# Performance work log

Measured on AMD Instinct MI355X. Metric: run time of the kernel, lower is better.

The kernel has to match this reference:

```python
import jax, jax.numpy as jnp
import numpy as np


def phi(x):
    # ELU + 1 feature map (Katharopoulos et al. 2020)
    return jax.nn.elu(x) + 1.0


def setup_inputs() -> dict:
    key = jax.random.key(0)
    k1, k2, k3 = jax.random.split(key, 3)
    B, T, D = 2, 2048, 512
    x = jax.random.normal(k1, (B, T, D), dtype=jnp.float32)
    # torch nn.Linear stores weight as (out_features, in_features)
    w_qkv = jax.random.normal(k2, (3 * D, D), dtype=jnp.float32) * 0.02
    w_out = jax.random.normal(k3, (D, D), dtype=jnp.float32) * 0.02
    return {"x": x, "w_qkv": w_qkv, "w_out": w_out, "n_heads": 16}


def reference(x, w_qkv, w_out, n_heads):
    B, T, D = x.shape
    H = n_heads
    Dh = D // H
    qkv = x @ w_qkv.T                                   # (B,T,3D)
    qkv = qkv.reshape(B, T, 3, H, Dh).transpose(2, 0, 3, 1, 4)  # (3,B,H,T,Dh)
    q, k, v = phi(qkv[0]), phi(qkv[1]), qkv[2]
    # kv outer product: (B,H,T,Dh_k,Dh_v), causal cumsum over time
    kv = k[..., :, None] * v[..., None, :]
    kv_cumsum = jnp.cumsum(kv, axis=2)
    num = jnp.einsum('bhtd,bhtde->bhte', q, kv_cumsum)  # (B,H,T,Dh)
    k_cumsum = jnp.cumsum(k, axis=2)
    denom = jnp.einsum('bhtd,bhtd->bht', q, k_cumsum)[..., None]
    denom = jnp.maximum(denom, 1e-6)
    out = num / denom                                   # (B,H,T,Dh)
    out = out.transpose(0, 2, 1, 3).reshape(B, T, D)
    return out @ w_out.T
```

## Files before the change

### kernel.cpp

```cpp
#include <hip/hip_runtime.h>
#include <math.h>

#define B_ 2
#define T_ 2048
#define D_ 512
#define H_ 16
#define DH 32
#define L_ 64
#define C_ 32
#define BH 32
#define NC 1024
#define VTP 72

typedef __attribute__((ext_vector_type(8))) short bf16x8;
typedef __attribute__((ext_vector_type(4))) float f32x4;
typedef __attribute__((ext_vector_type(4))) unsigned short u16x4;

#define AS1 __attribute__((address_space(1)))
#define AS3 __attribute__((address_space(3)))

__device__ __forceinline__ float bf2f(unsigned short u) {
    union { float f; unsigned int i; } v; v.i = ((unsigned int)u) << 16; return v.f;
}
__device__ __forceinline__ unsigned short f2bf(float f) {
    union { float f; unsigned int u; } v; v.f = f;
    unsigned int u = v.u;
    unsigned int r = u + 0x7FFFu + ((u >> 16) & 1u);
    return (unsigned short)(r >> 16);
}
__device__ __forceinline__ bf16x8 phi_frag(bf16x8 in) {
    bf16x8 r;
    #pragma unroll
    for (int i = 0; i < 8; ++i) {
        float f = bf2f((unsigned short)in[i]);
        f = f > 0.f ? f + 1.f : __expf(f);
        r[i] = (short)f2bf(f);
    }
    return r;
}
__device__ __forceinline__ void gload_lds16(const unsigned short* g, unsigned short* l) {
    __builtin_amdgcn_global_load_lds((const AS1 unsigned int*)g, (AS3 unsigned int*)l, 16, 0, 0);
}

__global__ __launch_bounds__(256) void convert_all(const float* __restrict__ x,
                                                   const float* __restrict__ wq,
                                                   const float* __restrict__ wo,
                                                   unsigned short* __restrict__ xb,
                                                   unsigned short* __restrict__ wqb,
                                                   unsigned short* __restrict__ wob)
{
    int i = blockIdx.x * 256 + threadIdx.x;
    const float* src; unsigned short* dst; int off;
    if (i < 524288)      { src = x;  dst = xb;  off = i; }
    else if (i < 720896) { src = wq; dst = wqb; off = i - 524288; }
    else                 { src = wo; dst = wob; off = i - 720896; }
    float4 v = ((const float4*)src)[off];
    u16x4 o;
    o.x = f2bf(v.x); o.y = f2bf(v.y); o.z = f2bf(v.z); o.w = f2bf(v.w);
    ((u16x4*)dst)[off] = o;
}

template<int BM, bool OUT_BF16>
__global__ __launch_bounds__(256) void gemm_bf16_nt(const unsigned short* __restrict__ A,
                                                    const unsigned short* __restrict__ W,
                                                    void* __restrict__ Cout,
                                                    int M, int N, int K)
{
    constexpr int MF = BM / 32;
    __shared__ unsigned short As[2][BM][32];
    __shared__ unsigned short Bs[2][128][32];
    const int tid = threadIdx.x;
    const int lane = tid & 63;
    const int wave = tid >> 6;
    const int wr = wave >> 1;
    const int wc = wave & 1;
    const size_t bm = (size_t)blockIdx.x * BM;
    const size_t bn = (size_t)blockIdx.y * 128;

    const int lrow = lane >> 2;
    const int lcol = (lane & 3) * 8;
    const unsigned short* ag0 = A + (bm + wave * (BM / 4) + lrow) * (size_t)K + lcol;
    const unsigned short* bg0 = W + (bn + wave * 32 + lrow) * (size_t)K + lcol;
    const unsigned short* bg1 = bg0 + (size_t)16 * K;

    auto stage = [&](int buf, int k0) {
        gload_lds16(ag0 + k0, &As[buf][wave * (BM / 4)][0]);
        if constexpr (BM == 128) gload_lds16(ag0 + (size_t)16 * K + k0, &As[buf][wave * (BM / 4) + 16][0]);
        gload_lds16(bg0 + k0, &Bs[buf][wave * 32][0]);
        gload_lds16(bg1 + k0, &Bs[buf][wave * 32 + 16][0]);
    };

    f32x4 acc[MF][4];
    #pragma unroll
    for (int m = 0; m < MF; ++m)
        #pragma unroll
        for (int n = 0; n < 4; ++n)
            acc[m][n] = (f32x4){0.f, 0.f, 0.f, 0.f};

    const int rr = lane & 15;
    const int kb = (lane >> 4) * 8;

    stage(0, 0);
    __syncthreads();
    int cur = 0;
    for (int k0 = 0; k0 < K; k0 += 32) {
        if (k0 + 32 < K) stage(cur ^ 1, k0 + 32);
        bf16x8 af[MF], bfr[4];
        #pragma unroll
        for (int m = 0; m < MF; ++m) af[m] = *(const bf16x8*)&As[cur][wr * (BM / 2) + m * 16 + rr][kb];
        #pragma unroll
        for (int n = 0; n < 4; ++n) bfr[n] = *(const bf16x8*)&Bs[cur][wc * 64 + n * 16 + rr][kb];
        #pragma unroll
        for (int m = 0; m < MF; ++m)
            #pragma unroll
            for (int n = 0; n < 4; ++n)
                acc[m][n] = __builtin_amdgcn_mfma_f32_16x16x32_bf16(af[m], bfr[n], acc[m][n], 0, 0, 0);
        __syncthreads();
        cur ^= 1;
    }

    const int cr = (lane >> 4) * 4;
    const int cc = lane & 15;
    #pragma unroll
    for (int m = 0; m < MF; ++m)
        #pragma unroll
        for (int n = 0; n < 4; ++n)
            #pragma unroll
            for (int j = 0; j < 4; ++j) {
                size_t row = bm + wr * (BM / 2) + m * 16 + cr + j;
                size_t col = bn + wc * 64 + n * 16 + cc;
                float v = acc[m][n][j];
                if (OUT_BF16) ((unsigned short*)Cout)[row * N + col] = f2bf(v);
                else          ((float*)Cout)[row * N + col] = v;
            }
}

__global__ __launch_bounds__(256) void chunk_sum(const unsigned short* __restrict__ qkv,
                                                 float* __restrict__ cSf)
{
    __shared__ unsigned short Kt[4][DH][VTP];
    __shared__ unsigned short Vt[4][48][VTP];
    const int tid = threadIdx.x;
    const int lane = tid & 63;
    const int wave = tid >> 6;
    const int chunk = blockIdx.x * 4 + wave;
    const int c = chunk & 31;
    const int h = (chunk >> 5) & 15;
    const int b = chunk >> 9;
    const size_t rowbase = ((size_t)(b * T_ + c * L_)) * (3 * D_) + h * DH;
    const int half = lane & 1;

    #pragma unroll
    for (int it = 0; it < 2; ++it) {
        int t = (lane >> 1) + it * 32;
        const unsigned short* kp = qkv + rowbase + (size_t)t * (3 * D_) + D_ + half * 16;
        const unsigned short* vp = qkv + rowbase + (size_t)t * (3 * D_) + 2 * D_ + half * 16;
        bf16x8 k0 = phi_frag(*(const bf16x8*)kp);
        bf16x8 k1 = phi_frag(*(const bf16x8*)(kp + 8));
        bf16x8 v0 = *(const bf16x8*)vp;
        bf16x8 v1 = *(const bf16x8*)(vp + 8);
        #pragma unroll
        for (int i = 0; i < 8; ++i) {
            Kt[wave][half * 16 + i][t]     = (unsigned short)k0[i];
            Kt[wave][half * 16 + 8 + i][t] = (unsigned short)k1[i];
            Vt[wave][half * 16 + i][t]     = (unsigned short)v0[i];
            Vt[wave][half * 16 + 8 + i][t] = (unsigned short)v1[i];
        }
    }
    Vt[wave][32][lane] = 0x3F80;

    const int fr = lane & 15;
    const int fg = lane >> 4;
    f32x4 acc[3][2];
    #pragma unroll
    for (int m = 0; m < 3; ++m)
        #pragma unroll
        for (int n = 0; n < 2; ++n)
            acc[m][n] = (f32x4){0.f, 0.f, 0.f, 0.f};

    #pragma unroll
    for (int ks = 0; ks < 2; ++ks) {
        int toff = fg * 8 + ks * 32;
        bf16x8 av[3], bk[2];
        #pragma unroll
        for (int m = 0; m < 3; ++m) av[m] = *(const bf16x8*)&Vt[wave][m * 16 + fr][toff];
        #pragma unroll
        for (int n = 0; n < 2; ++n) bk[n] = *(const bf16x8*)&Kt[wave][n * 16 + fr][toff];
        #pragma unroll
        for (int m = 0; m < 3; ++m)
            #pragma unroll
            for (int n = 0; n < 2; ++n)
                acc[m][n] = __builtin_amdgcn_mfma_f32_16x16x32_bf16(av[m], bk[n], acc[m][n], 0, 0, 0);
    }

    float* outp = cSf + (size_t)chunk * (48 * 32);
    #pragma unroll
    for (int m = 0; m < 2; ++m)
        #pragma unroll
        for (int n = 0; n < 2; ++n)
            #pragma unroll
            for (int r = 0; r < 4; ++r)
                outp[(m * 16 + fg * 4 + r) * 32 + n * 16 + fr] = acc[m][n][r];
    if (fg == 0) {
        #pragma unroll
        for (int n = 0; n < 2; ++n)
            outp[32 * 32 + n * 16 + fr] = acc[2][n][0];
    }
}

__global__ __launch_bounds__(256) void chunk_scan(const float* __restrict__ cSf,
                                                  unsigned short* __restrict__ cSt)
{
    int idx = blockIdx.x * 256 + threadIdx.x;
    int bh = idx / (33 * 32);
    int r  = idx % (33 * 32);
    const float* src = cSf + (size_t)bh * C_ * (48 * 32) + r;
    unsigned short* dst = cSt + (size_t)bh * C_ * (48 * 32) + r;
    float v[C_];
    #pragma unroll
    for (int c = 0; c < C_; ++c) v[c] = src[(size_t)c * (48 * 32)];
    float acc = 0.f;
    #pragma unroll
    for (int c = 0; c < C_; ++c) {
        dst[(size_t)c * (48 * 32)] = f2bf(acc);
        acc += v[c];
    }
}

__global__ __launch_bounds__(256) void chunk_out(const unsigned short* __restrict__ qkv,
                                                 const unsigned short* __restrict__ cSt,
                                                 unsigned short* __restrict__ attn)
{
    __shared__ unsigned short Vt[2][48][VTP];
    __shared__ unsigned short Am[4][32][VTP];
    const int tid = threadIdx.x;
    const int lane = tid & 63;
    const int wave = tid >> 6;
    const int ci = wave >> 1;
    const int wh = wave & 1;
    const int chunk = blockIdx.x * 2 + ci;
    const int c = chunk & 31;
    const int h = (chunk >> 5) & 15;
    const int b = chunk >> 9;
    const size_t rowbase = ((size_t)(b * T_ + c * L_)) * (3 * D_) + h * DH;
    const int fr = lane & 15;
    const int fg = lane >> 4;

    {
        int t = wh * 32 + (lane >> 1);
        int half = lane & 1;
        const unsigned short* vp = qkv + rowbase + (size_t)t * (3 * D_) + 2 * D_ + half * 16;
        bf16x8 v0 = *(const bf16x8*)vp;
        bf16x8 v1 = *(const bf16x8*)(vp + 8);
        #pragma unroll
        for (int i = 0; i < 8; ++i) {
            Vt[ci][half * 16 + i][t]     = (unsigned short)v0[i];
            Vt[ci][half * 16 + 8 + i][t] = (unsigned short)v1[i];
        }
        if (half == 0) Vt[ci][32][t] = 0x3F80;
    }

    bf16x8 aq[2];
    #pragma unroll
    for (int mm = 0; mm < 2; ++mm) {
        int m = wh * 2 + mm;
        const unsigned short* qp = qkv + rowbase + (size_t)(m * 16 + fr) * (3 * D_) + fg * 8;
        aq[mm] = phi_frag(*(const bf16x8*)qp);
    }
    bf16x8 bk[4];
    const int nmax = wh * 2 + 1;
    #pragma unroll
    for (int n = 0; n < 4; ++n) {
        if (n <= nmax) {
            const unsigned short* kp = qkv + rowbase + (size_t)(n * 16 + fr) * (3 * D_) + D_ + fg * 8;
            bk[n] = phi_frag(*(const bf16x8*)kp);
        }
    }
    bf16x8 bkv[3];
    #pragma unroll
    for (int n = 0; n < 3; ++n)
        bkv[n] = *(const bf16x8*)&cSt[(size_t)chunk * 1536 + (size_t)(n * 16 + fr) * 32 + fg * 8];

    f32x4 zero = (f32x4){0.f, 0.f, 0.f, 0.f};
    f32x4 acc[2][3];
    #pragma unroll
    for (int mm = 0; mm < 2; ++mm)
        #pragma unroll
        for (int n = 0; n < 3; ++n)
            acc[mm][n] = __builtin_amdgcn_mfma_f32_16x16x32_bf16(aq[mm], bkv[n], zero, 0, 0, 0);

    #pragma unroll
    for (int mm = 0; mm < 2; ++mm) {
        int m = wh * 2 + mm;
        #pragma unroll
        for (int n = 0; n < 4; ++n) {
            if (n <= m) {
                f32x4 s = __builtin_amdgcn_mfma_f32_16x16x32_bf16(aq[mm], bk[n], zero, 0, 0, 0);
                #pragma unroll
                for (int r = 0; r < 4; ++r) {
                    unsigned short v = f2bf(s[r]);
                    if (n == m && fr > fg * 4 + r) v = 0;
                    Am[wave][mm * 16 + fg * 4 + r][n * 16 + fr] = v;
                }
            }
        }
    }
    {
        int zc = wh ? 48 : 16;
        *(uint2*)&Am[wave][fr][zc + fg * 4] = (uint2){0u, 0u};
    }
    __syncthreads();

    #pragma unroll
    for (int ks = 0; ks < 2; ++ks) {
        if (ks <= wh) {
            bf16x8 bv[3];
            #pragma unroll
            for (int n = 0; n < 3; ++n)
                bv[n] = *(const bf16x8*)&Vt[ci][n * 16 + fr][fg * 8 + ks * 32];
            #pragma unroll
            for (int mm = 0; mm < 2; ++mm) {
                bf16x8 aa = *(const bf16x8*)&Am[wave][mm * 16 + fr][fg * 8 + ks * 32];
                #pragma unroll
                for (int n = 0; n < 3; ++n)
                    acc[mm][n] = __builtin_amdgcn_mfma_f32_16x16x32_bf16(aa, bv[n], acc[mm][n], 0, 0, 0);
            }
        }
    }

    #pragma unroll
    for (int mm = 0; mm < 2; ++mm) {
        float dn[4];
        #pragma unroll
        for (int r = 0; r < 4; ++r)
            dn[r] = __shfl(acc[mm][2][r], lane & 48);
        #pragma unroll
        for (int r = 0; r < 4; ++r) {
            float inv = 1.0f / fmaxf(dn[r], 1e-6f);
            #pragma unroll
            for (int n = 0; n < 2; ++n)
                Am[wave][mm * 16 + fg * 4 + r][n * 16 + fr] = f2bf(acc[mm][n][r] * inv);
        }
    }
    {
        int lrow = lane >> 1;
        int half = lane & 1;
        uint4 q0 = *(const uint4*)&Am[wave][lrow][half * 16];
        uint4 q1 = *(const uint4*)&Am[wave][lrow][half * 16 + 8];
        size_t grow = (size_t)(b * T_ + c * L_ + wh * 32 + lrow);
        unsigned short* dst = attn + grow * D_ + h * DH + half * 16;
        *(uint4*)dst = q0;
        *(uint4*)(dst + 8) = q1;
    }
}

extern "C" void kernel_launch(void* const* d_in, const int* in_sizes, int n_in,
                              void* d_out, int out_size, void* d_ws, size_t ws_size,
                              hipStream_t stream) {
    const float* x     = (const float*)d_in[0];
    const float* w_qkv = (const float*)d_in[1];
    const float* w_out = (const float*)d_in[2];
    float* out = (float*)d_out;

    char* ws = (char*)d_ws;
    unsigned short* qkvb  = (unsigned short*)ws;
    unsigned short* attnb = (unsigned short*)(ws + 12582912);
    unsigned short* xb    = (unsigned short*)(ws + 16777216);
    unsigned short* wqb   = (unsigned short*)(ws + 20971520);
    unsigned short* wob   = (unsigned short*)(ws + 22544384);
    float* cSf            = (float*)(ws + 23068672);
    unsigned short* cSt   = (unsigned short*)(ws + 29360128);

    convert_all<<<3072, 256, 0, stream>>>(x, w_qkv, w_out, xb, wqb, wob);

    dim3 g1(4096 / 128, 1536 / 128);
    gemm_bf16_nt<128, true><<<g1, 256, 0, stream>>>(xb, wqb, qkvb, 4096, 1536, 512);

    chunk_sum<<<NC / 4, 256, 0, stream>>>(qkvb, cSf);
    chunk_scan<<<132, 256, 0, stream>>>(cSf, cSt);
    chunk_out<<<NC / 2, 256, 0, stream>>>(qkvb, cSt, attnb);

    dim3 g2(4096 / 64, 512 / 128);
    gemm_bf16_nt<64, false><<<g2, 256, 0, stream>>>(attnb, wob, out, 4096, 512, 512);
}
```

Before: 52.27 us.

## Fuse fp32-to-bf16 conversion into GEMM tile staging, drop convert kernel

Removes the separate conversion kernel that wrote bf16 copies of x, w_qkv and w_out, and instead has both GEMMs load fp32 tiles into registers, convert them to bf16, and write them to LDS after the MFMA work of the current step. This saves one launch plus a full extra read and write of the inputs in global memory. In exchange, the GEMMs now read twice as many bytes per tile, lose the asynchronous global-to-LDS path for converted operands, and take on register pressure and conversion ALU work inside the main loop. Weights are reconverted by every block that uses them.

Result: faster. 48.84 us (-6.6%).

```diff
diff --git a/kernel.cpp b/kernel.cpp
--- a/kernel.cpp
+++ b/kernel.cpp
@@ -1,4 +1,5 @@
 #include <hip/hip_runtime.h>
+#include <hip/hip_bf16.h>
 #include <math.h>
 
 #define B_ 2
@@ -8,7 +9,6 @@
 #define DH 32
 #define L_ 64
 #define C_ 32
-#define BH 32
 #define NC 1024
 #define VTP 72
 
@@ -28,6 +28,10 @@
     unsigned int r = u + 0x7FFFu + ((u >> 16) & 1u);
     return (unsigned short)(r >> 16);
 }
+__device__ __forceinline__ unsigned short f2bf_rne(float f) {
+    __hip_bfloat16 h = __float2bfloat16(f);
+    union { __hip_bfloat16 h; unsigned short u; } v; v.h = h; return v.u;
+}
 __device__ __forceinline__ bf16x8 phi_frag(bf16x8 in) {
     bf16x8 r;
     #pragma unroll
@@ -42,31 +46,14 @@
     __builtin_amdgcn_global_load_lds((const AS1 unsigned int*)g, (AS3 unsigned int*)l, 16, 0, 0);
 }
 
-__global__ __launch_bounds__(256) void convert_all(const float* __restrict__ x,
-                                                   const float* __restrict__ wq,
-                                                   const float* __restrict__ wo,
-                                                   unsigned short* __restrict__ xb,
-                                                   unsigned short* __restrict__ wqb,
-                                                   unsigned short* __restrict__ wob)
-{
-    int i = blockIdx.x * 256 + threadIdx.x;
-    const float* src; unsigned short* dst; int off;
-    if (i < 524288)      { src = x;  dst = xb;  off = i; }
-    else if (i < 720896) { src = wq; dst = wqb; off = i - 524288; }
-    else                 { src = wo; dst = wob; off = i - 720896; }
-    float4 v = ((const float4*)src)[off];
-    u16x4 o;
-    o.x = f2bf(v.x); o.y = f2bf(v.y); o.z = f2bf(v.z); o.w = f2bf(v.w);
-    ((u16x4*)dst)[off] = o;
-}
-
-template<int BM, bool OUT_BF16>
-__global__ __launch_bounds__(256) void gemm_bf16_nt(const unsigned short* __restrict__ A,
-                                                    const unsigned short* __restrict__ W,
-                                                    void* __restrict__ Cout,
-                                                    int M, int N, int K)
+template<int BM, bool AF32, bool OUT_BF16>
+__global__ __launch_bounds__(256) void gemm_nt(const void* __restrict__ Aptr,
+                                               const float* __restrict__ Wf,
+                                               void* __restrict__ Cout,
+                                               int N, int K)
 {
     constexpr int MF = BM / 32;
+    constexpr int AF4 = BM / 32;
     __shared__ unsigned short As[2][BM][32];
     __shared__ unsigned short Bs[2][128][32];
     const int tid = threadIdx.x;
@@ -77,17 +64,51 @@
     const size_t bm = (size_t)blockIdx.x * BM;
     const size_t bn = (size_t)blockIdx.y * 128;
 
+    const int r8 = lane >> 3;
+    const int c4 = (lane & 7) * 4;
     const int lrow = lane >> 2;
     const int lcol = (lane & 3) * 8;
-    const unsigned short* ag0 = A + (bm + wave * (BM / 4) + lrow) * (size_t)K + lcol;
-    const unsigned short* bg0 = W + (bn + wave * 32 + lrow) * (size_t)K + lcol;
-    const unsigned short* bg1 = bg0 + (size_t)16 * K;
-
-    auto stage = [&](int buf, int k0) {
-        gload_lds16(ag0 + k0, &As[buf][wave * (BM / 4)][0]);
-        if constexpr (BM == 128) gload_lds16(ag0 + (size_t)16 * K + k0, &As[buf][wave * (BM / 4) + 16][0]);
-        gload_lds16(bg0 + k0, &Bs[buf][wave * 32][0]);
-        gload_lds16(bg1 + k0, &Bs[buf][wave * 32 + 16][0]);
+
+    const float* agf = nullptr;
+    const unsigned short* agb = nullptr;
+    if constexpr (AF32) agf = (const float*)Aptr + (bm + wave * (BM / 4) + r8) * (size_t)K + c4;
+    else                agb = (const unsigned short*)Aptr + (bm + wave * (BM / 4) + lrow) * (size_t)K + lcol;
+    const float* wgf = Wf + (bn + wave * 32 + r8) * (size_t)K + c4;
+
+    f32x4 aL[AF4];
+    f32x4 wL[4];
+
+    auto load_stage = [&](int buf, int k0) {
+        if constexpr (AF32) {
+            #pragma unroll
+            for (int i = 0; i < AF4; ++i)
+                aL[i] = *(const f32x4*)(agf + k0 + (size_t)(i * 8) * K);
+        } else {
+            gload_lds16(agb + k0, &As[buf][wave * (BM / 4)][0]);
+            if constexpr (BM / 4 == 32)
+                gload_lds16(agb + (size_t)16 * K + k0, &As[buf][wave * (BM / 4) + 16][0]);
+        }
+        #pragma unroll
+        for (int i = 0; i < 4; ++i)
+            wL[i] = *(const f32x4*)(wgf + k0 + (size_t)(i * 8) * K);
+    };
+    auto write_stage = [&](int buf) {
+        if constexpr (AF32) {
+            #pragma unroll
+            for (int i = 0; i < AF4; ++i) {
+                u16x4 o;
+                o.x = f2bf_rne(aL[i][0]); o.y = f2bf_rne(aL[i][1]);
+                o.z = f2bf_rne(aL[i][2]); o.w = f2bf_rne(aL[i][3]);
+                *(u16x4*)&As[buf][wave * (BM / 4) + r8 + i * 8][c4] = o;
+            }
+        }
+        #pragma unroll
+        for (int i = 0; i < 4; ++i) {
+            u16x4 o;
+            o.x = f2bf_rne(wL[i][0]); o.y = f2bf_rne(wL[i][1]);
+            o.z = f2bf_rne(wL[i][2]); o.w = f2bf_rne(wL[i][3]);
+            *(u16x4*)&Bs[buf][wave * 32 + r8 + i * 8][c4] = o;
+        }
     };
 
     f32x4 acc[MF][4];
@@ -100,21 +121,26 @@
     const int rr = lane & 15;
     const int kb = (lane >> 4) * 8;
 
-    stage(0, 0);
+    load_stage(0, 0);
+    write_stage(0);
     __syncthreads();
     int cur = 0;
     for (int k0 = 0; k0 < K; k0 += 32) {
-        if (k0 + 32 < K) stage(cur ^ 1, k0 + 32);
+        const bool more = k0 + 32 < K;
+        if (more) load_stage(cur ^ 1, k0 + 32);
         bf16x8 af[MF], bfr[4];
         #pragma unroll
-        for (int m = 0; m < MF; ++m) af[m] = *(const bf16x8*)&As[cur][wr * (BM / 2) + m * 16 + rr][kb];
-        #pragma unroll
-        for (int n = 0; n < 4; ++n) bfr[n] = *(const bf16x8*)&Bs[cur][wc * 64 + n * 16 + rr][kb];
+        for (int m = 0; m < MF; ++m)
+            af[m] = *(const bf16x8*)&As[cur][wr * (BM / 2) + m * 16 + rr][kb];
+        #pragma unroll
+        for (int n = 0; n < 4; ++n)
+            bfr[n] = *(const bf16x8*)&Bs[cur][wc * 64 + n * 16 + rr][kb];
         #pragma unroll
         for (int m = 0; m < MF; ++m)
             #pragma unroll
             for (int n = 0; n < 4; ++n)
                 acc[m][n] = __builtin_amdgcn_mfma_f32_16x16x32_bf16(af[m], bfr[n], acc[m][n], 0, 0, 0);
+        if (more) write_stage(cur ^ 1);
         __syncthreads();
         cur ^= 1;
     }
@@ -365,21 +391,18 @@
     char* ws = (char*)d_ws;
     unsigned short* qkvb  = (unsigned short*)ws;
     unsigned short* attnb = (unsigned short*)(ws + 12582912);
-    unsigned short* xb    = (unsigned short*)(ws + 16777216);
-    unsigned short* wqb   = (unsigned short*)(ws + 20971520);
-    unsigned short* wob   = (unsigned short*)(ws + 22544384);
-    float* cSf            = (float*)(ws + 23068672);
-    unsigned short* cSt   = (unsigned short*)(ws + 29360128);
-
-    convert_all<<<3072, 256, 0, stream>>>(x, w_qkv, w_out, xb, wqb, wob);
-
-    dim3 g1(4096 / 128, 1536 / 128);
-    gemm_bf16_nt<128, true><<<g1, 256, 0, stream>>>(xb, wqb, qkvb, 4096, 1536, 512);
+    float* cSf            = (float*)(ws + 16777216);
+    unsigned short* cSt   = (unsigned short*)(ws + 23068672);
+
+    gemm_nt<128, true, true><<<dim3(4096 / 128, 1536 / 128), 256, 0, stream>>>(
+        x, w_qkv, qkvb, 1536, 512);
 
     chunk_sum<<<NC / 4, 256, 0, stream>>>(qkvb, cSf);
+
     chunk_scan<<<132, 256, 0, stream>>>(cSf, cSt);
+
     chunk_out<<<NC / 2, 256, 0, stream>>>(qkvb, cSt, attnb);
 
-    dim3 g2(4096 / 64, 512 / 128);
-    gemm_bf16_nt<64, false><<<g2, 256, 0, stream>>>(attnb, wob, out, 4096, 512, 512);
-}
+    gemm_nt<64, false, false><<<dim3(4096 / 64, 512 / 128), 256, 0, stream>>>(
+        attnb, w_out, out, 512, 512);
+}
```
